# Kernel tuning notes

Hardware: AMD Instinct MI355X
Metric: run time of the kernel (lower is better)

Reference implementation:

```python
import jax, jax.numpy as jnp
import numpy as np
import math

N_EMBD = 1024
NUM_HEADS = 16
HEAD_DIM = N_EMBD // NUM_HEADS


def alibi_slopes(num_heads):
    x = (2 ** 8) ** (1.0 / num_heads)
    return jnp.array([1.0 / x ** (i + 1) for i in range(num_heads)], dtype=jnp.float32)


def setup_inputs() -> dict:
    key = jax.random.key(0)
    k1, k2 = jax.random.split(key)
    x = jax.random.normal(k1, (2, 2048, N_EMBD), dtype=jnp.float32)
    W_kqv = jax.random.normal(k2, (3 * N_EMBD, N_EMBD), dtype=jnp.float32) * (1.0 / math.sqrt(N_EMBD))
    return {"x": x, "W_kqv": W_kqv}


def reference(x, W_kqv):
    B, S, E = x.shape
    H, D = NUM_HEADS, HEAD_DIM
    kqv = jnp.einsum('bse,fe->bsf', x, W_kqv)  # Linear without bias
    k, q, v = jnp.split(kqv, 3, axis=-1)       # chunk order: key, query, value
    # [B, H, S, D]
    q = q.reshape(B, S, H, D).transpose(0, 2, 1, 3)
    k = k.reshape(B, S, H, D).transpose(0, 2, 1, 3)
    v = v.reshape(B, S, H, D).transpose(0, 2, 1, 3)
    # ALiBi bias: slopes[h] * (j - i), shape [H, S, S]
    rel = jnp.arange(S)[None, :] - jnp.arange(S)[:, None]  # [S, S]
    bias = alibi_slopes(H)[:, None, None] * rel.astype(jnp.float32)
    scale = math.sqrt(E)  # NOTE: module scales by sqrt(n_embd), not sqrt(head_dim)
    score = jnp.einsum('bhqd,bhkd->bhqk', q, k) / scale + bias[None]
    causal = jnp.tril(jnp.ones((S, S), dtype=bool))
    score = jnp.where(causal[None, None], score, -jnp.inf)
    attn = jax.nn.softmax(score, axis=-1)
    out = jnp.einsum('bhqk,bhkd->bhqd', attn, v)
    return out.transpose(0, 2, 1, 3).reshape(B, S, E)
```

## Files before the change

kernel.cpp:

```cpp
#include <hip/hip_runtime.h>
#include <hip/hip_bf16.h>
#include <math.h>

#define TOTAL_B 2
#define SEQ 2048
#define EMB 1024
#define NH 16
#define HD 64
#define M_GEMM (TOTAL_B*SEQ)
#define N_GEMM (3*EMB)
#define K_GEMM EMB

typedef __attribute__((ext_vector_type(8))) short short8;
typedef __attribute__((ext_vector_type(4))) float f32x4;
typedef __attribute__((ext_vector_type(4))) unsigned u32x4;

static __device__ __forceinline__ short f2bf(float f) {
  union { float f; unsigned u; } v; v.f = f;
  unsigned r = v.u + 0x7fff + ((v.u >> 16) & 1u);
  return (short)(r >> 16);
}

static __device__ __forceinline__ void gload_lds16(const void* g, void* l) {
  __builtin_amdgcn_global_load_lds(
      (const __attribute__((address_space(1))) void*)(uintptr_t)g,
      (__attribute__((address_space(3))) void*)(uintptr_t)l, 16, 0, 0);
}

static __device__ __forceinline__ float exp2v(float x) {
  float r; asm("v_exp_f32 %0, %1" : "=v"(r) : "v"(x)); return r;
}
static __device__ __forceinline__ unsigned cvtpk(float lo, float hi) {
  unsigned r; asm("v_cvt_pk_bf16_f32 %0, %1, %2" : "=v"(r) : "v"(lo), "v"(hi)); return r;
}
static __device__ __forceinline__ void pl32swap(unsigned &a, unsigned &b) {
  asm("v_permlane32_swap_b32 %0, %1" : "+v"(a), "+v"(b));
}

__global__ void cvt_kernel(const float* __restrict__ x, const float* __restrict__ w,
                           short* __restrict__ xb, short* __restrict__ wb) {
  const long nx = (long)M_GEMM * K_GEMM;
  const long nw = (long)N_GEMM * K_GEMM;
  long i = (long)blockIdx.x * blockDim.x + threadIdx.x;
  const long tot = (nx + nw) / 8;
  if (i >= tot) return;
  long e = i * 8;
  const float* s; short* d;
  if (e < nx) { s = x + e; d = xb + e; }
  else        { s = w + (e - nx); d = wb + (e - nx); }
  float4 a = ((const float4*)s)[0];
  float4 b = ((const float4*)s)[1];
  short8 o;
  o[0]=f2bf(a.x); o[1]=f2bf(a.y); o[2]=f2bf(a.z); o[3]=f2bf(a.w);
  o[4]=f2bf(b.x); o[5]=f2bf(b.y); o[6]=f2bf(b.z); o[7]=f2bf(b.w);
  *(short8*)d = o;
}

__global__ __launch_bounds__(512, 2) void qkv_gemm(const short* __restrict__ A, const short* __restrict__ Bm,
                                                   short* __restrict__ Kb, short* __restrict__ Qb,
                                                   short* __restrict__ Vb) {
  __shared__ __align__(16) short lds[57344];
  const int tid = threadIdx.x;
  const int lane = tid & 63;
  const int wid = tid >> 6;
  const int lr = lane & 15, lg = lane >> 4;
  const int m0 = blockIdx.y * 256, n0 = blockIdx.x * 192;
  const int wr = wid >> 1;
  const int wc = wid & 1;
  const int srcRow = tid >> 3;
  const int srcCh  = (tid & 7) ^ (srcRow & 7);

  f32x4 acc[4][6] = {};

  auto stageA = [&](int buf, int kt, int u) {
    const int row = u*64 + srcRow;
    gload_lds16(A + (size_t)(m0 + row)*K_GEMM + kt*64 + srcCh*8,
                &lds[buf*16384 + u*4096 + tid*8]);
  };
  auto stageB = [&](int buf, int kt, int u) {
    const int row = u*64 + srcRow;
    gload_lds16(Bm + (size_t)(n0 + row)*K_GEMM + kt*64 + srcCh*8,
                &lds[32768 + buf*12288 + u*4096 + tid*8]);
  };
  auto readA = [&](int buf, int mi, int kk) -> short8 {
    const int r = wr*64 + mi*16 + lr;
    const int c = (kk*4 + lg) ^ (r & 7);
    return *(const short8*)(&lds[buf*16384 + r*64 + c*8]);
  };
  auto readB = [&](int buf, int nj, int kk) -> short8 {
    const int r = wc*96 + nj*16 + lr;
    const int c = (kk*4 + lg) ^ (r & 7);
    return *(const short8*)(&lds[32768 + buf*12288 + r*64 + c*8]);
  };

#pragma unroll
  for (int u = 0; u < 4; ++u) stageA(0, 0, u);
#pragma unroll
  for (int u = 0; u < 3; ++u) stageB(0, 0, u);
  asm volatile("s_waitcnt vmcnt(0)" ::: "memory");
  __builtin_amdgcn_s_barrier();

  short8 aq[2][2], bq[6][2];
  const int NT = K_GEMM / 64;
#pragma unroll 1
  for (int kt = 0; kt < NT; ++kt) {
    const int buf = kt & 1, nb = buf ^ 1;
    const bool more = (kt + 1 < NT);

#pragma unroll
    for (int kk = 0; kk < 2; ++kk) {
      aq[0][kk] = readA(buf, 0, kk); aq[1][kk] = readA(buf, 1, kk);
      bq[0][kk] = readB(buf, 0, kk); bq[1][kk] = readB(buf, 1, kk); bq[2][kk] = readB(buf, 2, kk);
    }
    if (more) { stageA(nb, kt+1, 0); stageA(nb, kt+1, 1); }
    __builtin_amdgcn_s_barrier();
    asm volatile("s_waitcnt lgkmcnt(0)" ::: "memory");
    __builtin_amdgcn_sched_barrier(0);
    __builtin_amdgcn_s_setprio(1);
#pragma unroll
    for (int mi = 0; mi < 2; ++mi)
#pragma unroll
      for (int nj = 0; nj < 3; ++nj)
#pragma unroll
        for (int kk = 0; kk < 2; ++kk)
          acc[mi][nj] = __builtin_amdgcn_mfma_f32_16x16x32_bf16(aq[mi][kk], bq[nj][kk], acc[mi][nj], 0, 0, 0);
    __builtin_amdgcn_s_setprio(0);
    __builtin_amdgcn_sched_barrier(0);
    __builtin_amdgcn_s_barrier();

#pragma unroll
    for (int kk = 0; kk < 2; ++kk) {
      bq[3][kk] = readB(buf, 3, kk); bq[4][kk] = readB(buf, 4, kk); bq[5][kk] = readB(buf, 5, kk);
    }
    if (more) { stageA(nb, kt+1, 2); stageA(nb, kt+1, 3); }
    __builtin_amdgcn_s_barrier();
    asm volatile("s_waitcnt lgkmcnt(0)" ::: "memory");
    __builtin_amdgcn_sched_barrier(0);
    __builtin_amdgcn_s_setprio(1);
#pragma unroll
    for (int mi = 0; mi < 2; ++mi)
#pragma unroll
      for (int nj = 3; nj < 6; ++nj)
#pragma unroll
        for (int kk = 0; kk < 2; ++kk)
          acc[mi][nj] = __builtin_amdgcn_mfma_f32_16x16x32_bf16(aq[mi][kk], bq[nj][kk], acc[mi][nj], 0, 0, 0);
    __builtin_amdgcn_s_setprio(0);
    __builtin_amdgcn_sched_barrier(0);
    __builtin_amdgcn_s_barrier();

#pragma unroll
    for (int kk = 0; kk < 2; ++kk) {
      aq[0][kk] = readA(buf, 2, kk); aq[1][kk] = readA(buf, 3, kk);
    }
    if (more) { stageB(nb, kt+1, 0); stageB(nb, kt+1, 1); }
    __builtin_amdgcn_s_barrier();
    asm volatile("s_waitcnt lgkmcnt(0)" ::: "memory");
    __builtin_amdgcn_sched_barrier(0);
    __builtin_amdgcn_s_setprio(1);
#pragma unroll
    for (int mi = 0; mi < 2; ++mi)
#pragma unroll
      for (int nj = 3; nj < 6; ++nj)
#pragma unroll
        for (int kk = 0; kk < 2; ++kk)
          acc[mi+2][nj] = __builtin_amdgcn_mfma_f32_16x16x32_bf16(aq[mi][kk], bq[nj][kk], acc[mi+2][nj], 0, 0, 0);
    __builtin_amdgcn_s_setprio(0);
    __builtin_amdgcn_sched_barrier(0);
    __builtin_amdgcn_s_barrier();

#pragma unroll
    for (int kk = 0; kk < 2; ++kk) {
      bq[0][kk] = readB(buf, 0, kk); bq[1][kk] = readB(buf, 1, kk); bq[2][kk] = readB(buf, 2, kk);
    }
    if (more) { stageB(nb, kt+1, 2); }
    __builtin_amdgcn_s_barrier();
    asm volatile("s_waitcnt lgkmcnt(0)" ::: "memory");
    __builtin_amdgcn_sched_barrier(0);
    __builtin_amdgcn_s_setprio(1);
#pragma unroll
    for (int mi = 0; mi < 2; ++mi)
#pragma unroll
      for (int nj = 0; nj < 3; ++nj)
#pragma unroll
        for (int kk = 0; kk < 2; ++kk)
          acc[mi+2][nj] = __builtin_amdgcn_mfma_f32_16x16x32_bf16(aq[mi][kk], bq[nj][kk], acc[mi+2][nj], 0, 0, 0);
    __builtin_amdgcn_s_setprio(0);
    __builtin_amdgcn_sched_barrier(0);

    asm volatile("s_waitcnt vmcnt(0)" ::: "memory");
    __builtin_amdgcn_s_barrier();
  }

#pragma unroll
  for (int nj = 0; nj < 6; ++nj) {
    const int f = n0 + wc*96 + nj*16 + lr;
    const int which = f >> 10, fl = f & 1023;
    const int h = fl >> 6, d = fl & 63;
    short* dst = (which == 0) ? Kb : (which == 1) ? Qb : Vb;
    const float scale = (which == 1) ? 0.04508422f : 1.0f;
    short* base = dst + (size_t)h*SEQ*HD + d;
#pragma unroll
    for (int mi = 0; mi < 4; ++mi)
#pragma unroll
      for (int r = 0; r < 4; ++r) {
        const int m = m0 + wr*64 + mi*16 + lg*4 + r;
        const int b = m >> 11, s = m & 2047;
        base[((size_t)b*NH*SEQ + s)*HD] = f2bf(acc[mi][nj][r] * scale);
      }
  }
}

__global__ void vtrans(const short* __restrict__ Vb, short* __restrict__ Vt) {
  __shared__ short t[64][72];
  const int hb = blockIdx.y;
  const int s0 = blockIdx.x * 64;
  const short* src = Vb + ((size_t)hb*SEQ + s0)*HD;
  short* dst = Vt + (size_t)hb*HD*SEQ;
  const int tid = threadIdx.x;
#pragma unroll
  for (int i = 0; i < 2; ++i) {
    const int e = i*2048 + tid*8;
    const int r = e >> 6, c = e & 63;
    short8 v = *(const short8*)(src + (size_t)r*HD + c);
#pragma unroll
    for (int j = 0; j < 8; ++j) t[r][c+j] = v[j];
  }
  __syncthreads();
#pragma unroll
  for (int i = 0; i < 2; ++i) {
    const int e = i*2048 + tid*8;
    const int d = e >> 6, ss = e & 63;
    short8 v;
#pragma unroll
    for (int j = 0; j < 8; ++j) v[j] = t[ss+j][d];
    *(short8*)(dst + (size_t)d*SEQ + s0 + ss) = v;
  }
}

__global__ __launch_bounds__(256, 4) void attn_kernel(const short* __restrict__ Kb, const short* __restrict__ Qb,
                                                      const short* __restrict__ Vt, float* __restrict__ Out) {
  __shared__ __align__(16) short Ks[3][64*64];
  __shared__ __align__(16) short Vs[2][64*64];
  const int tid = threadIdx.x, lane = tid & 63, wid = tid >> 6;
  const int lr = lane & 15, lg = lane >> 4;
  const int bh = blockIdx.x;
  const int b = bh >> 4, h = bh & 15;
  const int qt = 31 - blockIdx.y;
  const float slope = exp2f(-0.5f * (float)(h + 1)) * 1.44269504f;
  const short* Kp = Kb + (size_t)bh * SEQ * HD;
  const short* Qp = Qb + (size_t)bh * SEQ * HD;
  const short* Vp = Vt + (size_t)bh * HD * SEQ;
  float* Ob = Out + (size_t)b * SEQ * EMB + (size_t)h * HD;

  const int q0 = qt * 64, qrb = q0 + wid * 16;
  const int nt = qt + 1;

  short8 qf[2];
#pragma unroll
  for (int kk = 0; kk < 2; ++kk)
    qf[kk] = *(const short8*)(Qp + (size_t)(qrb + lr)*HD + kk*32 + lg*8);

  const int bp = ((lr & 4) << 1) | ((lr & 2) << 1) | ((lr & 8) >> 2) | (lr & 1);
  const int cbase = qrb + lr - ((lg & 1) * 8 + (lg >> 1) * 2);

  float m_run = -INFINITY, l_run = 0.f;
  f32x4 o[4] = {};

  auto stageK = [&](int buf, int t) {
    const int kv0 = t * 64;
#pragma unroll
    for (int i = 0; i < 2; ++i) {
      const int e16 = i*256 + tid;
      const int row = e16 >> 3, ch = e16 & 7;
      const int sch = ch ^ (row & 7);
      gload_lds16(Kp + (size_t)(kv0 + row)*HD + sch*8, &Ks[buf][i*2048 + wid*512]);
    }
  };
  auto stageV = [&](int buf, int t) {
    const int kv0 = t * 64;
#pragma unroll
    for (int i = 0; i < 2; ++i) {
      const int e16 = i*256 + tid;
      const int row = e16 >> 3, ch = e16 & 7;
      const int sch = ch ^ (row & 7);
      gload_lds16(Vp + (size_t)row*SEQ + kv0 + sch*8, &Vs[buf][i*2048 + wid*512]);
    }
  };
  auto qkt = [&](int buf, f32x4* sc) {
    short8 kf[4][2];
#pragma unroll
    for (int kvf = 0; kvf < 4; ++kvf) {
      const int row = kvf*16 + bp;
#pragma unroll
      for (int kk = 0; kk < 2; ++kk) {
        const int c = (kk*4 + lg) ^ (row & 7);
        kf[kvf][kk] = *(const short8*)(&Ks[buf][row*64 + c*8]);
      }
    }
    __builtin_amdgcn_s_setprio(1);
#pragma unroll
    for (int kvf = 0; kvf < 4; ++kvf) {
      f32x4 s = {};
      s = __builtin_amdgcn_mfma_f32_16x16x32_bf16(kf[kvf][0], qf[0], s, 0, 0, 0);
      s = __builtin_amdgcn_mfma_f32_16x16x32_bf16(kf[kvf][1], qf[1], s, 0, 0, 0);
      sc[kvf] = s;
    }
    __builtin_amdgcn_s_setprio(0);
  };

  stageK(0, 0);
  if (nt > 1) stageK(1, 1);
  stageV(0, 0);
  __syncthreads();
  f32x4 sc_cur[4], sc_next[4];
  qkt(0, sc_cur);

  int k1 = 1, k2 = 2;
#pragma unroll 1
  for (int t = 0; t < nt; ++t) {
    const int kv0 = t * 64;
    if (t + 2 < nt) stageK(k2, t + 2);
    if (t + 1 < nt) stageV((t + 1) & 1, t + 1);
    if (t + 1 < nt) qkt(k1, sc_next);

    const float dbase = (float)(kv0 - cbase);
    float v[4][4];
    if (t == nt - 1) {
#pragma unroll
      for (int kvf = 0; kvf < 4; ++kvf)
#pragma unroll
        for (int r = 0; r < 4; ++r) {
          const float C = (float)(kvf*16 + (r>>1)*4 + (r&1));
          const float toff = dbase + C;
          float val = fmaf(slope, toff, sc_cur[kvf][r]);
          if (toff > 0.f) val = -INFINITY;
          v[kvf][r] = val;
        }
    } else {
#pragma unroll
      for (int kvf = 0; kvf < 4; ++kvf)
#pragma unroll
        for (int r = 0; r < 4; ++r) {
          const float C = (float)(kvf*16 + (r>>1)*4 + (r&1));
          v[kvf][r] = fmaf(slope, dbase + C, sc_cur[kvf][r]);
        }
    }
    float q0m = fmaxf(fmaxf(v[0][0], v[0][1]), fmaxf(v[0][2], v[0][3]));
    float q1m = fmaxf(fmaxf(v[1][0], v[1][1]), fmaxf(v[1][2], v[1][3]));
    float q2m = fmaxf(fmaxf(v[2][0], v[2][1]), fmaxf(v[2][2], v[2][3]));
    float q3m = fmaxf(fmaxf(v[3][0], v[3][1]), fmaxf(v[3][2], v[3][3]));
    float mt = fmaxf(fmaxf(q0m, q1m), fmaxf(q2m, q3m));
    mt = fmaxf(mt, __shfl_xor(mt, 16, 64));
    mt = fmaxf(mt, __shfl_xor(mt, 32, 64));

    if (__any(mt > m_run + 10.f)) {
      const float mn = fmaxf(m_run, mt);
      const float corr = exp2v(m_run - mn);
      m_run = mn;
      l_run *= corr;
      float co[4];
#pragma unroll
      for (int r = 0; r < 4; ++r) co[r] = __shfl(corr, lg*4 + r, 64);
#pragma unroll
      for (int dt = 0; dt < 4; ++dt)
#pragma unroll
        for (int r = 0; r < 4; ++r) o[dt][r] *= co[r];
    }
#pragma unroll
    for (int kvf = 0; kvf < 4; ++kvf)
#pragma unroll
      for (int r = 0; r < 4; ++r)
        v[kvf][r] = exp2v(v[kvf][r] - m_run);
    float s0 = (v[0][0]+v[0][1]) + (v[0][2]+v[0][3]);
    float s1 = (v[1][0]+v[1][1]) + (v[1][2]+v[1][3]);
    float s2 = (v[2][0]+v[2][1]) + (v[2][2]+v[2][3]);
    float s3 = (v[3][0]+v[3][1]) + (v[3][2]+v[3][3]);
    float lt = (s0+s1) + (s2+s3);
    lt += __shfl_xor(lt, 16, 64);
    lt += __shfl_xor(lt, 32, 64);
    l_run += lt;

    unsigned pk[4][2];
#pragma unroll
    for (int kvf = 0; kvf < 4; ++kvf) {
      pk[kvf][0] = cvtpk(v[kvf][0], v[kvf][1]);
      pk[kvf][1] = cvtpk(v[kvf][2], v[kvf][3]);
    }
    __builtin_amdgcn_s_setprio(1);
#pragma unroll
    for (int ks = 0; ks < 2; ++ks) {
      unsigned w0 = pk[2*ks][0], w1 = pk[2*ks+1][0];
      pl32swap(w0, w1);
      unsigned w2 = pk[2*ks][1], w3 = pk[2*ks+1][1];
      pl32swap(w2, w3);
      u32x4 wv = {w0, w1, w2, w3};
      const short8 pf = __builtin_bit_cast(short8, wv);
#pragma unroll
      for (int dt = 0; dt < 4; ++dt) {
        const int rv = dt*16 + lr;
        const int cv = (ks*4 + lg) ^ (rv & 7);
        const short8 vf = *(const short8*)(&Vs[t & 1][rv*64 + cv*8]);
        o[dt] = __builtin_amdgcn_mfma_f32_16x16x32_bf16(pf, vf, o[dt], 0, 0, 0);
      }
    }
    __builtin_amdgcn_s_setprio(0);

    __syncthreads();
#pragma unroll
    for (int kvf = 0; kvf < 4; ++kvf) sc_cur[kvf] = sc_next[kvf];
    k1 = k2; k2 = (k2 == 2) ? 0 : k2 + 1;
  }

  const float inv = 1.f / l_run;
  float li[4];
#pragma unroll
  for (int r = 0; r < 4; ++r) li[r] = __shfl(inv, lg*4 + r, 64);
#pragma unroll
  for (int dt = 0; dt < 4; ++dt)
#pragma unroll
    for (int r = 0; r < 4; ++r) {
      const int iq = qrb + lg*4 + r;
      Ob[(size_t)iq*EMB + dt*16 + lr] = o[dt][r] * li[r];
    }
}

extern "C" void kernel_launch(void* const* d_in, const int* in_sizes, int n_in,
                              void* d_out, int out_size, void* d_ws, size_t ws_size,
                              hipStream_t stream) {
  const float* x = (const float*)d_in[0];
  const float* w = (const float*)d_in[1];
  char* ws = (char*)d_ws;
  if (ws_size < 39845888u) return;
  short* xb = (short*)(ws);
  short* wb = (short*)(ws + 8388608u);
  short* Kb = (short*)(ws + 14680064u);
  short* Qb = (short*)(ws + 23068672u);
  short* Vb = (short*)(ws + 31457280u);
  short* Vt = xb;
  float* out = (float*)d_out;

  cvt_kernel<<<3584, 256, 0, stream>>>(x, w, xb, wb);
  qkv_gemm<<<dim3(N_GEMM/192, M_GEMM/256), 512, 0, stream>>>(xb, wb, Kb, Qb, Vb);
  vtrans<<<dim3(SEQ/64, TOTAL_B*NH), 256, 0, stream>>>(Vb, Vt);
  attn_kernel<<<dim3(TOTAL_B*NH, 32), 256, 0, stream>>>(Kb, Qb, Vt, out);
}
```

Baseline: 92.76 us.

## Load V fragments straight from global and look ahead on softmax max

```diff
diff --git a/kernel.cpp b/kernel.cpp
--- a/kernel.cpp
+++ b/kernel.cpp
@@ -239,8 +239,7 @@
 
 __global__ __launch_bounds__(256, 4) void attn_kernel(const short* __restrict__ Kb, const short* __restrict__ Qb,
                                                       const short* __restrict__ Vt, float* __restrict__ Out) {
-  __shared__ __align__(16) short Ks[3][64*64];
-  __shared__ __align__(16) short Vs[2][64*64];
+  __shared__ __align__(16) short Ks[2][64*64];
   const int tid = threadIdx.x, lane = tid & 63, wid = tid >> 6;
   const int lr = lane & 15, lg = lane >> 4;
   const int bh = blockIdx.x;
@@ -276,16 +275,6 @@
       gload_lds16(Kp + (size_t)(kv0 + row)*HD + sch*8, &Ks[buf][i*2048 + wid*512]);
     }
   };
-  auto stageV = [&](int buf, int t) {
-    const int kv0 = t * 64;
-#pragma unroll
-    for (int i = 0; i < 2; ++i) {
-      const int e16 = i*256 + tid;
-      const int row = e16 >> 3, ch = e16 & 7;
-      const int sch = ch ^ (row & 7);
-      gload_lds16(Vp + (size_t)row*SEQ + kv0 + sch*8, &Vs[buf][i*2048 + wid*512]);
-    }
-  };
   auto qkt = [&](int buf, f32x4* sc) {
     short8 kf[4][2];
 #pragma unroll
@@ -307,74 +296,87 @@
     }
     __builtin_amdgcn_s_setprio(0);
   };
+  auto biasmax = [&](int tt, const f32x4* sc, float vv[4][4]) -> float {
+    const float dbase = (float)(tt*64 - cbase);
+    if (tt == nt - 1) {
+#pragma unroll
+      for (int kvf = 0; kvf < 4; ++kvf)
+#pragma unroll
+        for (int r = 0; r < 4; ++r) {
+          const float C = (float)(kvf*16 + (r>>1)*4 + (r&1));
+          const float toff = dbase + C;
+          float val = fmaf(slope, toff, sc[kvf][r]);
+          if (toff > 0.f) val = -INFINITY;
+          vv[kvf][r] = val;
+        }
+    } else {
+#pragma unroll
+      for (int kvf = 0; kvf < 4; ++kvf)
+#pragma unroll
+        for (int r = 0; r < 4; ++r) {
+          const float C = (float)(kvf*16 + (r>>1)*4 + (r&1));
+          vv[kvf][r] = fmaf(slope, dbase + C, sc[kvf][r]);
+        }
+    }
+    float a0 = fmaxf(fmaxf(vv[0][0], vv[0][1]), fmaxf(vv[0][2], vv[0][3]));
+    float a1 = fmaxf(fmaxf(vv[1][0], vv[1][1]), fmaxf(vv[1][2], vv[1][3]));
+    float a2 = fmaxf(fmaxf(vv[2][0], vv[2][1]), fmaxf(vv[2][2], vv[2][3]));
+    float a3 = fmaxf(fmaxf(vv[3][0], vv[3][1]), fmaxf(vv[3][2], vv[3][3]));
+    float mt = fmaxf(fmaxf(a0, a1), fmaxf(a2, a3));
+    mt = fmaxf(mt, __shfl_xor(mt, 16, 64));
+    mt = fmaxf(mt, __shfl_xor(mt, 32, 64));
+    return mt;
+  };
 
   stageK(0, 0);
   if (nt > 1) stageK(1, 1);
-  stageV(0, 0);
   __syncthreads();
-  f32x4 sc_cur[4], sc_next[4];
-  qkt(0, sc_cur);
-
-  int k1 = 1, k2 = 2;
+  f32x4 sc[4];
+  qkt(0, sc);
+  float vc[4][4];
+  m_run = biasmax(0, sc, vc);
+  __syncthreads();
+
 #pragma unroll 1
   for (int t = 0; t < nt; ++t) {
     const int kv0 = t * 64;
-    if (t + 2 < nt) stageK(k2, t + 2);
-    if (t + 1 < nt) stageV((t + 1) & 1, t + 1);
-    if (t + 1 < nt) qkt(k1, sc_next);
-
-    const float dbase = (float)(kv0 - cbase);
-    float v[4][4];
-    if (t == nt - 1) {
-#pragma unroll
-      for (int kvf = 0; kvf < 4; ++kvf)
-#pragma unroll
-        for (int r = 0; r < 4; ++r) {
-          const float C = (float)(kvf*16 + (r>>1)*4 + (r&1));
-          const float toff = dbase + C;
-          float val = fmaf(slope, toff, sc_cur[kvf][r]);
-          if (toff > 0.f) val = -INFINITY;
-          v[kvf][r] = val;
-        }
-    } else {
-#pragma unroll
-      for (int kvf = 0; kvf < 4; ++kvf)
-#pragma unroll
-        for (int r = 0; r < 4; ++r) {
-          const float C = (float)(kvf*16 + (r>>1)*4 + (r&1));
-          v[kvf][r] = fmaf(slope, dbase + C, sc_cur[kvf][r]);
-        }
-    }
-    float q0m = fmaxf(fmaxf(v[0][0], v[0][1]), fmaxf(v[0][2], v[0][3]));
-    float q1m = fmaxf(fmaxf(v[1][0], v[1][1]), fmaxf(v[1][2], v[1][3]));
-    float q2m = fmaxf(fmaxf(v[2][0], v[2][1]), fmaxf(v[2][2], v[2][3]));
-    float q3m = fmaxf(fmaxf(v[3][0], v[3][1]), fmaxf(v[3][2], v[3][3]));
-    float mt = fmaxf(fmaxf(q0m, q1m), fmaxf(q2m, q3m));
-    mt = fmaxf(mt, __shfl_xor(mt, 16, 64));
-    mt = fmaxf(mt, __shfl_xor(mt, 32, 64));
-
-    if (__any(mt > m_run + 10.f)) {
-      const float mn = fmaxf(m_run, mt);
-      const float corr = exp2v(m_run - mn);
-      m_run = mn;
-      l_run *= corr;
-      float co[4];
-#pragma unroll
-      for (int r = 0; r < 4; ++r) co[r] = __shfl(corr, lg*4 + r, 64);
-#pragma unroll
-      for (int dt = 0; dt < 4; ++dt)
-#pragma unroll
-        for (int r = 0; r < 4; ++r) o[dt][r] *= co[r];
-    }
+    short8 vf[8];
+#pragma unroll
+    for (int dt = 0; dt < 4; ++dt)
+#pragma unroll
+      for (int ks = 0; ks < 2; ++ks)
+        vf[dt*2 + ks] = *(const short8*)(Vp + (size_t)(dt*16 + lr)*SEQ + kv0 + ks*32 + lg*8);
+    if (t + 2 < nt) stageK(t & 1, t + 2);
+
+    float vn[4][4];
+    const bool have_next = (t + 1 < nt);
+    if (have_next) {
+      qkt((t + 1) & 1, sc);
+      const float mtn = biasmax(t + 1, sc, vn);
+      if (__any(mtn > m_run + 10.f)) {
+        const float mn = fmaxf(m_run, mtn);
+        const float corr = exp2v(m_run - mn);
+        m_run = mn;
+        l_run *= corr;
+        float co[4];
+#pragma unroll
+        for (int r = 0; r < 4; ++r) co[r] = __shfl(corr, lg*4 + r, 64);
+#pragma unroll
+        for (int dt = 0; dt < 4; ++dt)
+#pragma unroll
+          for (int r = 0; r < 4; ++r) o[dt][r] *= co[r];
+      }
+    }
+
 #pragma unroll
     for (int kvf = 0; kvf < 4; ++kvf)
 #pragma unroll
       for (int r = 0; r < 4; ++r)
-        v[kvf][r] = exp2v(v[kvf][r] - m_run);
-    float s0 = (v[0][0]+v[0][1]) + (v[0][2]+v[0][3]);
-    float s1 = (v[1][0]+v[1][1]) + (v[1][2]+v[1][3]);
-    float s2 = (v[2][0]+v[2][1]) + (v[2][2]+v[2][3]);
-    float s3 = (v[3][0]+v[3][1]) + (v[3][2]+v[3][3]);
+        vc[kvf][r] = exp2v(vc[kvf][r] - m_run);
+    float s0 = (vc[0][0]+vc[0][1]) + (vc[0][2]+vc[0][3]);
+    float s1 = (vc[1][0]+vc[1][1]) + (vc[1][2]+vc[1][3]);
+    float s2 = (vc[2][0]+vc[2][1]) + (vc[2][2]+vc[2][3]);
+    float s3 = (vc[3][0]+vc[3][1]) + (vc[3][2]+vc[3][3]);
     float lt = (s0+s1) + (s2+s3);
     lt += __shfl_xor(lt, 16, 64);
     lt += __shfl_xor(lt, 32, 64);
@@ -383,8 +385,8 @@
     unsigned pk[4][2];
 #pragma unroll
     for (int kvf = 0; kvf < 4; ++kvf) {
-      pk[kvf][0] = cvtpk(v[kvf][0], v[kvf][1]);
-      pk[kvf][1] = cvtpk(v[kvf][2], v[kvf][3]);
+      pk[kvf][0] = cvtpk(vc[kvf][0], vc[kvf][1]);
+      pk[kvf][1] = cvtpk(vc[kvf][2], vc[kvf][3]);
     }
     __builtin_amdgcn_s_setprio(1);
 #pragma unroll
@@ -396,19 +398,19 @@
       u32x4 wv = {w0, w1, w2, w3};
       const short8 pf = __builtin_bit_cast(short8, wv);
 #pragma unroll
-      for (int dt = 0; dt < 4; ++dt) {
-        const int rv = dt*16 + lr;
-        const int cv = (ks*4 + lg) ^ (rv & 7);
-        const short8 vf = *(const short8*)(&Vs[t & 1][rv*64 + cv*8]);
-        o[dt] = __builtin_amdgcn_mfma_f32_16x16x32_bf16(pf, vf, o[dt], 0, 0, 0);
-      }
+      for (int dt = 0; dt < 4; ++dt)
+        o[dt] = __builtin_amdgcn_mfma_f32_16x16x32_bf16(pf, vf[dt*2 + ks], o[dt], 0, 0, 0);
     }
     __builtin_amdgcn_s_setprio(0);
 
     __syncthreads();
-#pragma unroll
-    for (int kvf = 0; kvf < 4; ++kvf) sc_cur[kvf] = sc_next[kvf];
-    k1 = k2; k2 = (k2 == 2) ? 0 : k2 + 1;
+    if (have_next) {
+#pragma unroll
+      for (int kvf = 0; kvf < 4; ++kvf)
+#pragma unroll
+        for (int r = 0; r < 4; ++r)
+          vc[kvf][r] = vn[kvf][r];
+    }
   }
 
   const float inv = 1.f / l_run;
```

New measurement: 146.8 us. +58.2%, slower.
